# Kernel tuning notes

Hardware: AMD Instinct MI355X
Metric: run time of the kernel (lower is better)

## Reference

```python
import jax, jax.numpy as jnp
import numpy as np

N0, N1, N2 = 320000, 80000, 16000
E1, E2 = 800000, 160000
IN_C, HID, OUT_C = 128, 64, 48
H1, H2 = 4, 1
NEG_SLOPE = 0.2  # PyG GATv2Conv default leaky_relu slope


def _glorot(key, shape):
    fan_in = shape[0]
    return jax.random.normal(key, shape, jnp.float32) / jnp.sqrt(jnp.asarray(fan_in, jnp.float32))


def setup_inputs() -> dict:
    key = jax.random.key(0)
    ks = jax.random.split(key, 12)
    inp = {
        "x": jax.random.normal(ks[0], (N0, IN_C), jnp.float32),
        # layer 1: GATv2Conv(IN_C -> HID, heads=H1, concat=True)
        "Wl1": _glorot(ks[1], (IN_C, H1 * HID)),
        "bl1": jnp.zeros((H1 * HID,), jnp.float32),
        "Wr1": _glorot(ks[2], (IN_C, H1 * HID)),
        "br1": jnp.zeros((H1 * HID,), jnp.float32),
        "att1": jax.random.normal(ks[3], (H1, HID), jnp.float32) * 0.1,
        "bias1": jnp.zeros((H1 * HID,), jnp.float32),
        # layer 2: GATv2Conv(H1*HID -> OUT_C, heads=H2, concat=False)
        "Wl2": _glorot(ks[4], (H1 * HID, H2 * OUT_C)),
        "bl2": jnp.zeros((H2 * OUT_C,), jnp.float32),
        "Wr2": _glorot(ks[5], (H1 * HID, H2 * OUT_C)),
        "br2": jnp.zeros((H2 * OUT_C,), jnp.float32),
        "att2": jax.random.normal(ks[6], (H2, OUT_C), jnp.float32) * 0.1,
        "bias2": jnp.zeros((OUT_C,), jnp.float32),
        # sampled bipartite edge lists (edge j->i: src index into x_src, dst into x_dst)
        "src1": jax.random.randint(ks[7], (E1,), 0, N0, jnp.int32),
        "dst1": jax.random.randint(ks[8], (E1,), 0, N1, jnp.int32),
        "src2": jax.random.randint(ks[9], (E2,), 0, N1, jnp.int32),
        "dst2": jax.random.randint(ks[10], (E2,), 0, N2, jnp.int32),
        "n1": N1,
        "n2": N2,
    }
    return inp


def gatv2_conv(x_src, x_dst, src, dst, Wl, bl, Wr, br, att, bias, n_dst, concat):
    H, C = att.shape
    xl = (x_src @ Wl + bl).reshape(-1, H, C)   # [N_src, H, C] (source transform)
    xr = (x_dst @ Wr + br).reshape(-1, H, C)   # [N_dst, H, C] (target transform)
    e = xl[src] + xr[dst]                      # [E, H, C]
    e = jnp.where(e > 0, e, NEG_SLOPE * e)     # leaky_relu (GATv2: nonlinearity before att)
    alpha = jnp.einsum('ehc,hc->eh', e, att)   # [E, H] attention logits
    # softmax over edges sharing the same target node
    amax = jax.ops.segment_max(alpha, dst, num_segments=n_dst)
    ex = jnp.exp(alpha - amax[dst])
    denom = jax.ops.segment_sum(ex, dst, num_segments=n_dst)
    w = ex / (denom[dst] + 1e-16)              # [E, H]
    out = jax.ops.segment_sum(xl[src] * w[:, :, None], dst, num_segments=n_dst)  # [N_dst, H, C]
    out = out.reshape(n_dst, H * C) if concat else out.mean(axis=1)
    return out + bias


def reference(x, Wl1, bl1, Wr1, br1, att1, bias1, Wl2, bl2, Wr2, br2, att2, bias2,
              src1, dst1, src2, dst2, n1, n2):
    h = gatv2_conv(x, x[:n1], src1, dst1, Wl1, bl1, Wr1, br1, att1, bias1, n1, True)
    h = jax.nn.relu(h)
    # dropout is identity in eval mode
    h = gatv2_conv(h, h[:n2], src2, dst2, Wl2, bl2, Wr2, br2, att2, bias2, n2, False)
    return jax.nn.log_softmax(h, axis=-1)
```

## Files before the change

### kernel.cpp

```cpp
#include <hip/hip_runtime.h>
#include <hip/hip_bf16.h>

#define N0_  320000
#define N1_  80000
#define N2_  16000
#define INC_ 128
#define HID_ 64
#define H1_  4
#define C1_  256
#define OUT_ 48
#define OUTP_ 64
#define NEG_ 0.2f

typedef __attribute__((ext_vector_type(8))) short bfrag8;
typedef __attribute__((ext_vector_type(4))) float ffrag4;

__device__ __forceinline__ float bf2f(unsigned short u){
  unsigned int v = ((unsigned int)u) << 16;
  return __uint_as_float(v);
}
__device__ __forceinline__ unsigned short f2bf(float f){
  unsigned int u = __float_as_uint(f);
  u += 0x7FFFu + ((u >> 16) & 1u);
  return (unsigned short)(u >> 16);
}
__device__ __forceinline__ void unpack2(unsigned int u, float& lo, float& hi){
  lo = __uint_as_float(u << 16);
  hi = __uint_as_float(u & 0xffff0000u);
}

__global__ void transpose_all(const float* __restrict__ Wl1, const float* __restrict__ Wr1,
                              const float* __restrict__ Wl2, const float* __restrict__ Wr2,
                              unsigned short* __restrict__ Wt1l, unsigned short* __restrict__ Wt1r,
                              unsigned short* __restrict__ Wt2l, unsigned short* __restrict__ Wt2r){
  int idx = blockIdx.x*256 + threadIdx.x;
  if (idx < 32768){ int n = idx >> 7, k = idx & 127; Wt1l[idx] = f2bf(Wl1[k*C1_ + n]); }
  else if (idx < 65536){ int j = idx - 32768; int n = j >> 7, k = j & 127; Wt1r[j] = f2bf(Wr1[k*C1_ + n]); }
  else if (idx < 77824){ int j = idx - 65536; int n = j >> 8, k = j & 255; Wt2l[j] = f2bf(Wl2[k*OUT_ + n]); }
  else if (idx < 90112){ int j = idx - 77824; int n = j >> 8, k = j & 255; Wt2r[j] = f2bf(Wr2[k*OUT_ + n]); }
}

__global__ __launch_bounds__(256, 2) void gemm1_v4(
    const float* __restrict__ X,
    const unsigned short* __restrict__ Wtl, const unsigned short* __restrict__ Wtr,
    const float* __restrict__ bl, const float* __restrict__ br,
    unsigned short* __restrict__ outl, unsigned short* __restrict__ outr,
    int nblk_l, int tiles)
{
  __shared__ unsigned short As[64*136];
  __shared__ unsigned short Csh[32*264];
  const int t = threadIdx.x;
  const int lane = t & 63, wave = t >> 6;
  const bool isR = (int)blockIdx.x >= nblk_l;
  const int blk = isR ? (int)blockIdx.x - nblk_l : (int)blockIdx.x;
  const unsigned short* Wt = isR ? Wtr : Wtl;
  const float* bias = isR ? br : bl;
  unsigned short* out = isR ? outr : outl;
  const int l15 = lane & 15, q = lane >> 4;
  const int wcol = wave << 6;
  const int r8 = t >> 5;
  const int c32 = t & 31;

  int row0 = (blk * tiles) << 6;
  float4 pf[8];
  #pragma unroll
  for (int i = 0; i < 8; ++i)
    pf[i] = *(const float4*)(X + ((size_t)(row0 + (i<<3) + r8) << 7) + (c32<<2));

  bfrag8 bfr[4][4];
  #pragma unroll
  for (int nt = 0; nt < 4; ++nt)
    #pragma unroll
    for (int ks = 0; ks < 4; ++ks)
      bfr[nt][ks] = *(const bfrag8*)(Wt + (size_t)(wcol + (nt<<4) + l15)*128 + (ks<<5) + (q<<3));
  float bb[4];
  #pragma unroll
  for (int nt = 0; nt < 4; ++nt) bb[nt] = bias[wcol + (nt<<4) + l15];

  #pragma unroll
  for (int i = 0; i < 8; ++i){
    ushort4 s; s.x=f2bf(pf[i].x); s.y=f2bf(pf[i].y); s.z=f2bf(pf[i].z); s.w=f2bf(pf[i].w);
    *(ushort4*)(&As[((i<<3) + r8)*136 + (c32<<2)]) = s;
  }
  __syncthreads();

  for (int tile = 0; tile < tiles; ++tile){
    row0 = (blk * tiles + tile) << 6;
    const bool havenext = (tile + 1 < tiles);
    if (havenext){
      int rown = row0 + 64;
      #pragma unroll
      for (int i = 0; i < 8; ++i)
        pf[i] = *(const float4*)(X + ((size_t)(rown + (i<<3) + r8) << 7) + (c32<<2));
    }

    ffrag4 z = {0.f,0.f,0.f,0.f};
    ffrag4 acc[4][4];
    #pragma unroll
    for (int mt = 0; mt < 4; ++mt)
      #pragma unroll
      for (int nt = 0; nt < 4; ++nt) acc[mt][nt] = z;

    #pragma unroll
    for (int mt = 0; mt < 4; ++mt)
      #pragma unroll
      for (int ks = 0; ks < 4; ++ks){
        bfrag8 af = *(const bfrag8*)(&As[((mt<<4) + l15)*136 + (ks<<5) + (q<<3)]);
        #pragma unroll
        for (int nt = 0; nt < 4; ++nt)
          acc[mt][nt] = __builtin_amdgcn_mfma_f32_16x16x32_bf16(af, bfr[nt][ks], acc[mt][nt], 0, 0, 0);
      }

    __syncthreads();
    if (havenext){
      #pragma unroll
      for (int i = 0; i < 8; ++i){
        ushort4 s; s.x=f2bf(pf[i].x); s.y=f2bf(pf[i].y); s.z=f2bf(pf[i].z); s.w=f2bf(pf[i].w);
        *(ushort4*)(&As[((i<<3) + r8)*136 + (c32<<2)]) = s;
      }
    }

    #pragma unroll
    for (int h = 0; h < 2; ++h){
      if (h) __syncthreads();
      #pragma unroll
      for (int mh = 0; mh < 2; ++mh){
        int mt = (h<<1) + mh;
        #pragma unroll
        for (int nt = 0; nt < 4; ++nt)
          #pragma unroll
          for (int rg = 0; rg < 4; ++rg)
            Csh[((mh<<4) + (q<<2) + rg)*264 + wcol + (nt<<4) + l15] = f2bf(acc[mt][nt][rg] + bb[nt]);
      }
      __syncthreads();
      #pragma unroll
      for (int i = 0; i < 4; ++i){
        int idx = (i<<8) + t;
        int r = idx >> 5, c = (idx & 31) << 3;
        *(bfrag8*)(out + ((size_t)(row0 + (h<<5) + r) << 8) + c) = *(const bfrag8*)(&Csh[r*264 + c]);
      }
    }
    __syncthreads();
  }
}

__global__ __launch_bounds__(256) void gemm2_v2(
    const unsigned short* __restrict__ Hin,
    const unsigned short* __restrict__ Wtl, const unsigned short* __restrict__ Wtr,
    const float* __restrict__ bl, const float* __restrict__ br,
    float* __restrict__ outl, float* __restrict__ outr, int nblk_l)
{
  const int t = threadIdx.x;
  const int lane = t & 63, wave = t >> 6;
  const bool isR = (int)blockIdx.x >= nblk_l;
  const int row0 = (isR ? (int)blockIdx.x - nblk_l : (int)blockIdx.x) << 6;
  const unsigned short* Wt = isR ? Wtr : Wtl;
  const float* bias = isR ? br : bl;
  float* out = isR ? outr : outl;
  const int l15 = lane & 15, q = lane >> 4;

  if (wave < 3){
    bfrag8 bfr[8];
    #pragma unroll
    for (int ks = 0; ks < 8; ++ks)
      bfr[ks] = *(const bfrag8*)(Wt + (size_t)((wave<<4) + l15)*256 + (ks<<5) + (q<<3));
    ffrag4 z = {0.f,0.f,0.f,0.f};
    ffrag4 acc[4] = {z, z, z, z};
    #pragma unroll
    for (int ks = 0; ks < 8; ++ks){
      #pragma unroll
      for (int mt = 0; mt < 4; ++mt){
        bfrag8 af = *(const bfrag8*)(Hin + ((size_t)(row0 + (mt<<4) + l15) << 8) + (ks<<5) + (q<<3));
        acc[mt] = __builtin_amdgcn_mfma_f32_16x16x32_bf16(af, bfr[ks], acc[mt], 0, 0, 0);
      }
    }
    int col = (wave<<4) + l15;
    float bbv = bias[col];
    #pragma unroll
    for (int mt = 0; mt < 4; ++mt)
      #pragma unroll
      for (int rg = 0; rg < 4; ++rg){
        int row = row0 + (mt<<4) + (q<<2) + rg;
        out[(size_t)row*OUTP_ + col] = acc[mt][rg] + bbv;
      }
  } else {
    #pragma unroll
    for (int i = 0; i < 16; ++i){
      int row = row0 + (i<<2) + q;
      out[(size_t)row*OUTP_ + 48 + l15] = 0.f;
    }
  }
}

__global__ void hist_both(const int* __restrict__ dst1, const int* __restrict__ dst2,
                          int* __restrict__ cnt1, int* __restrict__ cnt2, int E1, int E2){
  int i = blockIdx.x*256 + threadIdx.x;
  if (i < E1) atomicAdd(&cnt1[dst1[i]], 1);
  else if (i < E1 + E2) atomicAdd(&cnt2[dst2[i - E1]], 1);
}

__global__ __launch_bounds__(256) void scan_local_both(
    const int* __restrict__ in1, const int* __restrict__ in2,
    int* __restrict__ ex1, int* __restrict__ ex2,
    int* __restrict__ part1, int* __restrict__ part2, int n1, int n2, int nb1){
  __shared__ int s[256];
  const int* in; int* excl; int* partials; int n; int b;
  if ((int)blockIdx.x < nb1){ in = in1; excl = ex1; partials = part1; n = n1; b = blockIdx.x; }
  else { in = in2; excl = ex2; partials = part2; n = n2; b = blockIdx.x - nb1; }
  int t = threadIdx.x, i = b*256 + t;
  int v = (i < n) ? in[i] : 0;
  s[t] = v; __syncthreads();
  #pragma unroll
  for (int off = 1; off < 256; off <<= 1){
    int u = (t >= off) ? s[t-off] : 0;
    __syncthreads();
    s[t] += u; __syncthreads();
  }
  if (i < n) excl[i] = s[t] - v;
  if (t == 255) partials[b] = s[255];
}

__global__ __launch_bounds__(512) void scan_partials_both(
    int* __restrict__ part1, int* __restrict__ part2, int nb1, int nb2){
  __shared__ int s[512];
  int* partials = blockIdx.x ? part2 : part1;
  int nb = blockIdx.x ? nb2 : nb1;
  int t = threadIdx.x;
  int v = (t < nb) ? partials[t] : 0;
  s[t] = v; __syncthreads();
  #pragma unroll
  for (int off = 1; off < 512; off <<= 1){
    int u = (t >= off) ? s[t-off] : 0;
    __syncthreads();
    s[t] += u; __syncthreads();
  }
  if (t < nb) partials[t] = s[t] - v;
}

__global__ void scan_finalize_both(
    int* __restrict__ ex1, int* __restrict__ ex2,
    const int* __restrict__ part1, const int* __restrict__ part2,
    int* __restrict__ cur1, int* __restrict__ cur2, int n1, int n2, int nb1){
  int* excl; const int* partials; int* cursor; int n; int b;
  if ((int)blockIdx.x < nb1){ excl = ex1; partials = part1; cursor = cur1; n = n1; b = blockIdx.x; }
  else { excl = ex2; partials = part2; cursor = cur2; n = n2; b = blockIdx.x - nb1; }
  int i = b*256 + threadIdx.x;
  if (i >= n) return;
  int o = excl[i] + partials[b];
  excl[i] = o; cursor[i] = o;
}

__global__ void scatter_both(const int* __restrict__ src1, const int* __restrict__ dst1,
                             const int* __restrict__ src2, const int* __restrict__ dst2,
                             int* __restrict__ cur1, int* __restrict__ cur2,
                             int* __restrict__ perm1, int* __restrict__ perm2, int E1, int E2){
  int i = blockIdx.x*256 + threadIdx.x;
  if (i < E1){
    int pos = atomicAdd(&cur1[dst1[i]], 1);
    perm1[pos] = src1[i];
  } else if (i < E1 + E2){
    int j = i - E1;
    int pos = atomicAdd(&cur2[dst2[j]], 1);
    perm2[pos] = src2[j];
  }
}

__global__ __launch_bounds__(256) void gat_aggregate1(
    const unsigned short* __restrict__ xl, const unsigned short* __restrict__ xr,
    const int* __restrict__ offsets, const int* __restrict__ counts,
    const int* __restrict__ perm, const float* __restrict__ att,
    const float* __restrict__ bias, unsigned short* __restrict__ hout, int n)
{
  int node = (blockIdx.x << 2) + (threadIdx.x >> 6);
  if (node >= n) return;
  const int lane = threadIdx.x & 63;
  const int slot = lane >> 5;
  const int sub  = lane & 31;
  const int elem = sub << 3;
  const unsigned int ebyte = (unsigned)elem << 1;
  const char* xlb = (const char*)xl;

  const int st = offsets[node], cnt = counts[node];
  uint4 ru = *(const uint4*)(xr + ((size_t)node << 8) + elem);
  float r[8];
  unpack2(ru.x, r[0], r[1]); unpack2(ru.y, r[2], r[3]);
  unpack2(ru.z, r[4], r[5]); unpack2(ru.w, r[6], r[7]);
  float4 al = *(const float4*)(att + elem);
  float4 ah = *(const float4*)(att + elem + 4);
  float a[8] = {al.x, al.y, al.z, al.w, ah.x, ah.y, ah.z, ah.w};

  float acc[8] = {0,0,0,0,0,0,0,0};
  float den = 0.f;

  for (int jb = 0; jb < cnt; jb += 64){
    int m = cnt - jb; if (m > 64) m = 64;
    int pv = (lane < m) ? perm[st + jb + lane] : 0;
    int s_cur = __shfl(pv, slot);
    uint4 xc = *(const uint4*)(xlb + (((unsigned)s_cur << 9) + ebyte));
    for (int j = 0; j < m; j += 2){
      int s_next = __shfl(pv, (j + 2 + slot) & 63);
      uint4 xn = *(const uint4*)(xlb + (((unsigned)s_next << 9) + ebyte));
      float x[8];
      unpack2(xc.x, x[0], x[1]); unpack2(xc.y, x[2], x[3]);
      unpack2(xc.z, x[4], x[5]); unpack2(xc.w, x[6], x[7]);
      float p = 0.f;
      #pragma unroll
      for (int i = 0; i < 8; ++i){
        float v = x[i] + r[i];
        float e = fmaf(NEG_, fminf(v, 0.f), fmaxf(v, 0.f));
        p = fmaf(e, a[i], p);
      }
      p += __shfl_xor(p, 1);
      p += __shfl_xor(p, 2);
      p += __shfl_xor(p, 4);
      float ex = __expf(p);
      ex = (j + slot < m) ? ex : 0.f;
      den += ex;
      #pragma unroll
      for (int i = 0; i < 8; ++i) acc[i] = fmaf(ex, x[i], acc[i]);
      xc = xn;
    }
  }
  den += __shfl_xor(den, 32);
  #pragma unroll
  for (int i = 0; i < 8; ++i) acc[i] += __shfl_xor(acc[i], 32);

  if (slot == 0){
    float w = 1.f / (den + 1e-16f);
    float4 bl = *(const float4*)(bias + elem);
    float4 bh = *(const float4*)(bias + elem + 4);
    float b[8] = {bl.x, bl.y, bl.z, bl.w, bh.x, bh.y, bh.z, bh.w};
    unsigned int o[4];
    #pragma unroll
    for (int i = 0; i < 4; ++i){
      unsigned short lo = f2bf(fmaxf(fmaf(acc[2*i],   w, b[2*i]),   0.f));
      unsigned short hi = f2bf(fmaxf(fmaf(acc[2*i+1], w, b[2*i+1]), 0.f));
      o[i] = (unsigned)lo | ((unsigned)hi << 16);
    }
    *(uint4*)(hout + ((size_t)node << 8) + elem) = make_uint4(o[0], o[1], o[2], o[3]);
  }
}

__global__ __launch_bounds__(256) void gat_aggregate2(
    const float* __restrict__ xl, const float* __restrict__ xr,
    const int* __restrict__ offsets, const int* __restrict__ counts,
    const int* __restrict__ perm, const float* __restrict__ att,
    const float* __restrict__ bias, float* __restrict__ out, int n)
{
  int node = (blockIdx.x << 2) + (threadIdx.x >> 6);
  if (node >= n) return;
  const int lane = threadIdx.x & 63;
  const int slot = lane >> 4;
  const int sub  = lane & 15;
  const bool realc = sub < 12;

  const int st = offsets[node], cnt = counts[node];
  float4 r = *(const float4*)(xr + (size_t)node*OUTP_ + (sub<<2));
  float4 a = realc ? *(const float4*)(att + (sub<<2)) : make_float4(0,0,0,0);
  float4 acc = make_float4(0,0,0,0);
  float den = 0.f;

  for (int jb = 0; jb < cnt; jb += 64){
    int m = cnt - jb; if (m > 64) m = 64;
    int pv = (lane < m) ? perm[st + jb + lane] : 0;
    int s_cur = __shfl(pv, slot);
    float4 xc = *(const float4*)(xl + (size_t)((unsigned)s_cur*OUTP_ + (sub<<2)));
    for (int j = 0; j < m; j += 4){
      int s_next = __shfl(pv, (j + 4 + slot) & 63);
      float4 xn = *(const float4*)(xl + (size_t)((unsigned)s_next*OUTP_ + (sub<<2)));
      float v0 = xc.x + r.x, v1 = xc.y + r.y, v2 = xc.z + r.z, v3 = xc.w + r.w;
      float p;
      p = fmaf(a.x, fmaf(NEG_, fminf(v0,0.f), fmaxf(v0,0.f)), 0.f);
      p = fmaf(a.y, fmaf(NEG_, fminf(v1,0.f), fmaxf(v1,0.f)), p);
      p = fmaf(a.z, fmaf(NEG_, fminf(v2,0.f), fmaxf(v2,0.f)), p);
      p = fmaf(a.w, fmaf(NEG_, fminf(v3,0.f), fmaxf(v3,0.f)), p);
      p += __shfl_xor(p, 1);
      p += __shfl_xor(p, 2);
      p += __shfl_xor(p, 4);
      p += __shfl_xor(p, 8);
      float ex = __expf(p);
      ex = (j + slot < m) ? ex : 0.f;
      den += ex;
      acc.x = fmaf(ex, xc.x, acc.x); acc.y = fmaf(ex, xc.y, acc.y);
      acc.z = fmaf(ex, xc.z, acc.z); acc.w = fmaf(ex, xc.w, acc.w);
      xc = xn;
    }
  }
  den += __shfl_xor(den, 16); den += __shfl_xor(den, 32);
  acc.x += __shfl_xor(acc.x, 16); acc.x += __shfl_xor(acc.x, 32);
  acc.y += __shfl_xor(acc.y, 16); acc.y += __shfl_xor(acc.y, 32);
  acc.z += __shfl_xor(acc.z, 16); acc.z += __shfl_xor(acc.z, 32);
  acc.w += __shfl_xor(acc.w, 16); acc.w += __shfl_xor(acc.w, 32);

  float w = 1.f / (den + 1e-16f);
  float4 b = realc ? *(const float4*)(bias + (sub<<2)) : make_float4(0,0,0,0);
  float v0 = fmaf(acc.x, w, b.x), v1 = fmaf(acc.y, w, b.y);
  float v2 = fmaf(acc.z, w, b.z), v3 = fmaf(acc.w, w, b.w);

  float mx = realc ? fmaxf(fmaxf(v0, v1), fmaxf(v2, v3)) : -3.0e38f;
  mx = fmaxf(mx, __shfl_xor(mx, 1)); mx = fmaxf(mx, __shfl_xor(mx, 2));
  mx = fmaxf(mx, __shfl_xor(mx, 4)); mx = fmaxf(mx, __shfl_xor(mx, 8));
  float es = realc ? (__expf(v0-mx) + __expf(v1-mx) + __expf(v2-mx) + __expf(v3-mx)) : 0.f;
  es += __shfl_xor(es, 1); es += __shfl_xor(es, 2);
  es += __shfl_xor(es, 4); es += __shfl_xor(es, 8);
  float ls = __logf(es);
  if (slot == 0 && realc){
    float4 o = make_float4(v0-mx-ls, v1-mx-ls, v2-mx-ls, v3-mx-ls);
    *(float4*)(out + (size_t)node*OUT_ + (sub<<2)) = o;
  }
}

extern "C" void kernel_launch(void* const* d_in, const int* in_sizes, int n_in,
                              void* d_out, int out_size, void* d_ws, size_t ws_size,
                              hipStream_t stream)
{
  const float* x    = (const float*)d_in[0];
  const float* Wl1  = (const float*)d_in[1];
  const float* bl1  = (const float*)d_in[2];
  const float* Wr1  = (const float*)d_in[3];
  const float* br1  = (const float*)d_in[4];
  const float* att1 = (const float*)d_in[5];
  const float* bias1= (const float*)d_in[6];
  const float* Wl2  = (const float*)d_in[7];
  const float* bl2  = (const float*)d_in[8];
  const float* Wr2  = (const float*)d_in[9];
  const float* br2  = (const float*)d_in[10];
  const float* att2 = (const float*)d_in[11];
  const float* bias2= (const float*)d_in[12];
  const int* src1 = (const int*)d_in[13];
  const int* dst1 = (const int*)d_in[14];
  const int* src2 = (const int*)d_in[15];
  const int* dst2 = (const int*)d_in[16];
  const int E1 = in_sizes[13];
  const int E2 = in_sizes[15];
  (void)n_in; (void)out_size; (void)ws_size;

  char* ws = (char*)d_ws;
  unsigned short* xl1  = (unsigned short*)(ws + 0LL);
  unsigned short* xr1  = (unsigned short*)(ws + 163840000LL);
  unsigned short* hbuf = (unsigned short*)(ws + 204800000LL);
  float* xl2p   = (float*)(ws + 245760000LL);
  float* xr2p   = (float*)(ws + 266240000LL);
  int*   perm1  = (int*)  (ws + 270336000LL);
  int*   perm2  = (int*)  (ws + 273536000LL);
  int*   cnt1   = (int*)  (ws + 274176000LL);
  int*   cnt2   = (int*)  (ws + 274496000LL);
  int*   off1   = (int*)  (ws + 274560000LL);
  int*   cur1   = (int*)  (ws + 274880000LL);
  int*   off2   = (int*)  (ws + 275200000LL);
  int*   cur2   = (int*)  (ws + 275264000LL);
  int*   part1  = (int*)  (ws + 275328000LL);
  int*   part2  = (int*)  (ws + 275330048LL);
  unsigned short* Wt1l = (unsigned short*)(ws + 275332096LL);
  unsigned short* Wt1r = (unsigned short*)(ws + 275397632LL);
  unsigned short* Wt2l = (unsigned short*)(ws + 275463168LL);
  unsigned short* Wt2r = (unsigned short*)(ws + 275487744LL);

  hipMemsetAsync(ws + 274176000LL, 0, 384000LL, stream);

  const int nb1 = (N1_ + 255) / 256;
  const int nb2 = (N2_ + 255) / 256;

  transpose_all<<<352, 256, 0, stream>>>(Wl1, Wr1, Wl2, Wr2, Wt1l, Wt1r, Wt2l, Wt2r);

  hist_both         <<<(E1+E2+255)/256, 256, 0, stream>>>(dst1, dst2, cnt1, cnt2, E1, E2);
  scan_local_both   <<<nb1+nb2, 256, 0, stream>>>(cnt1, cnt2, off1, off2, part1, part2, N1_, N2_, nb1);
  scan_partials_both<<<2, 512, 0, stream>>>(part1, part2, nb1, nb2);
  scan_finalize_both<<<nb1+nb2, 256, 0, stream>>>(off1, off2, part1, part2, cur1, cur2, N1_, N2_, nb1);
  scatter_both      <<<(E1+E2+255)/256, 256, 0, stream>>>(src1, dst1, src2, dst2,
                                                          cur1, cur2, perm1, perm2, E1, E2);

  gemm1_v4<<<1250, 256, 0, stream>>>(x, Wt1l, Wt1r, bl1, br1, xl1, xr1, 1000, 5);

  gat_aggregate1<<<(N1_+3)/4, 256, 0, stream>>>(xl1, xr1, off1, cnt1, perm1,
                                                att1, bias1, hbuf, N1_);

  gemm2_v2<<<N1_/64 + N2_/64, 256, 0, stream>>>(hbuf, Wt2l, Wt2r, bl2, br2, xl2p, xr2p, N1_/64);

  gat_aggregate2<<<(N2_+3)/4, 256, 0, stream>>>(xl2p, xr2p, off2, cnt2, perm2,
                                                att2, bias2, (float*)d_out, N2_);
}
```

Measured before the change: 553.5 us.

## Shrink gemm1 tile, store MFMA results directly, stage gemm2 A in LDS

gemm1 now works on 32-row tiles with twice as many blocks. The MFMA operands are swapped so each lane holds four consecutive output columns and can write bf16 results straight to global memory, which removes the shared-memory C staging and its extra barriers. gemm2 now stages the 64x256 input tile in LDS once, and each wave computes 16 rows across all 48 output columns with float4 stores, instead of three waves re-reading the input from global while one wave only writes zero padding. The cost is smaller per-block reuse in gemm1 and narrower 8-byte global stores.

```diff
diff --git a/kernel.cpp b/kernel.cpp
--- a/kernel.cpp
+++ b/kernel.cpp
@@ -40,15 +40,14 @@
   else if (idx < 90112){ int j = idx - 77824; int n = j >> 8, k = j & 255; Wt2r[j] = f2bf(Wr2[k*OUT_ + n]); }
 }
 
-__global__ __launch_bounds__(256, 2) void gemm1_v4(
+__global__ __launch_bounds__(256) void gemm1_v5(
     const float* __restrict__ X,
     const unsigned short* __restrict__ Wtl, const unsigned short* __restrict__ Wtr,
     const float* __restrict__ bl, const float* __restrict__ br,
     unsigned short* __restrict__ outl, unsigned short* __restrict__ outr,
     int nblk_l, int tiles)
 {
-  __shared__ unsigned short As[64*136];
-  __shared__ unsigned short Csh[32*264];
+  __shared__ unsigned short As[32*136];
   const int t = threadIdx.x;
   const int lane = t & 63, wave = t >> 6;
   const bool isR = (int)blockIdx.x >= nblk_l;
@@ -58,14 +57,6 @@
   unsigned short* out = isR ? outr : outl;
   const int l15 = lane & 15, q = lane >> 4;
   const int wcol = wave << 6;
-  const int r8 = t >> 5;
-  const int c32 = t & 31;
-
-  int row0 = (blk * tiles) << 6;
-  float4 pf[8];
-  #pragma unroll
-  for (int i = 0; i < 8; ++i)
-    pf[i] = *(const float4*)(X + ((size_t)(row0 + (i<<3) + r8) << 7) + (c32<<2));
 
   bfrag8 bfr[4][4];
   #pragma unroll
@@ -73,83 +64,89 @@
     #pragma unroll
     for (int ks = 0; ks < 4; ++ks)
       bfr[nt][ks] = *(const bfrag8*)(Wt + (size_t)(wcol + (nt<<4) + l15)*128 + (ks<<5) + (q<<3));
-  float bb[4];
-  #pragma unroll
-  for (int nt = 0; nt < 4; ++nt) bb[nt] = bias[wcol + (nt<<4) + l15];
-
-  #pragma unroll
-  for (int i = 0; i < 8; ++i){
+  float4 bb[4];
+  #pragma unroll
+  for (int nt = 0; nt < 4; ++nt)
+    bb[nt] = *(const float4*)(bias + wcol + (nt<<4) + (q<<2));
+
+  int row0 = (blk * tiles) << 5;
+  float4 pf[4];
+  #pragma unroll
+  for (int i = 0; i < 4; ++i){
+    int idx = (i<<8) + t;
+    pf[i] = *(const float4*)(X + ((size_t)(row0 + (idx>>5)) << 7) + ((idx&31)<<2));
+  }
+  #pragma unroll
+  for (int i = 0; i < 4; ++i){
+    int idx = (i<<8) + t;
     ushort4 s; s.x=f2bf(pf[i].x); s.y=f2bf(pf[i].y); s.z=f2bf(pf[i].z); s.w=f2bf(pf[i].w);
-    *(ushort4*)(&As[((i<<3) + r8)*136 + (c32<<2)]) = s;
+    *(ushort4*)(&As[(idx>>5)*136 + ((idx&31)<<2)]) = s;
   }
   __syncthreads();
 
   for (int tile = 0; tile < tiles; ++tile){
-    row0 = (blk * tiles + tile) << 6;
+    row0 = (blk * tiles + tile) << 5;
     const bool havenext = (tile + 1 < tiles);
     if (havenext){
-      int rown = row0 + 64;
-      #pragma unroll
-      for (int i = 0; i < 8; ++i)
-        pf[i] = *(const float4*)(X + ((size_t)(rown + (i<<3) + r8) << 7) + (c32<<2));
+      int rown = row0 + 32;
+      #pragma unroll
+      for (int i = 0; i < 4; ++i){
+        int idx = (i<<8) + t;
+        pf[i] = *(const float4*)(X + ((size_t)(rown + (idx>>5)) << 7) + ((idx&31)<<2));
+      }
     }
 
     ffrag4 z = {0.f,0.f,0.f,0.f};
-    ffrag4 acc[4][4];
-    #pragma unroll
-    for (int mt = 0; mt < 4; ++mt)
+    ffrag4 acc[2][4];
+    #pragma unroll
+    for (int mt = 0; mt < 2; ++mt)
       #pragma unroll
       for (int nt = 0; nt < 4; ++nt) acc[mt][nt] = z;
 
     #pragma unroll
-    for (int mt = 0; mt < 4; ++mt)
+    for (int mt = 0; mt < 2; ++mt)
       #pragma unroll
       for (int ks = 0; ks < 4; ++ks){
         bfrag8 af = *(const bfrag8*)(&As[((mt<<4) + l15)*136 + (ks<<5) + (q<<3)]);
         #pragma unroll
         for (int nt = 0; nt < 4; ++nt)
-          acc[mt][nt] = __builtin_amdgcn_mfma_f32_16x16x32_bf16(af, bfr[nt][ks], acc[mt][nt], 0, 0, 0);
+          acc[mt][nt] = __builtin_amdgcn_mfma_f32_16x16x32_bf16(bfr[nt][ks], af, acc[mt][nt], 0, 0, 0);
       }
+
+    #pragma unroll
+    for (int mt = 0; mt < 2; ++mt){
+      int row = row0 + (mt<<4) + l15;
+      #pragma unroll
+      for (int nt = 0; nt < 4; ++nt){
+        ushort4 s;
+        s.x = f2bf(acc[mt][nt][0] + bb[nt].x);
+        s.y = f2bf(acc[mt][nt][1] + bb[nt].y);
+        s.z = f2bf(acc[mt][nt][2] + bb[nt].z);
+        s.w = f2bf(acc[mt][nt][3] + bb[nt].w);
+        *(ushort4*)(out + ((size_t)row << 8) + wcol + (nt<<4) + (q<<2)) = s;
+      }
+    }
 
     __syncthreads();
     if (havenext){
       #pragma unroll
-      for (int i = 0; i < 8; ++i){
+      for (int i = 0; i < 4; ++i){
+        int idx = (i<<8) + t;
         ushort4 s; s.x=f2bf(pf[i].x); s.y=f2bf(pf[i].y); s.z=f2bf(pf[i].z); s.w=f2bf(pf[i].w);
-        *(ushort4*)(&As[((i<<3) + r8)*136 + (c32<<2)]) = s;
-      }
-    }
-
-    #pragma unroll
-    for (int h = 0; h < 2; ++h){
-      if (h) __syncthreads();
-      #pragma unroll
-      for (int mh = 0; mh < 2; ++mh){
-        int mt = (h<<1) + mh;
-        #pragma unroll
-        for (int nt = 0; nt < 4; ++nt)
-          #pragma unroll
-          for (int rg = 0; rg < 4; ++rg)
-            Csh[((mh<<4) + (q<<2) + rg)*264 + wcol + (nt<<4) + l15] = f2bf(acc[mt][nt][rg] + bb[nt]);
+        *(ushort4*)(&As[(idx>>5)*136 + ((idx&31)<<2)]) = s;
       }
       __syncthreads();
-      #pragma unroll
-      for (int i = 0; i < 4; ++i){
-        int idx = (i<<8) + t;
-        int r = idx >> 5, c = (idx & 31) << 3;
-        *(bfrag8*)(out + ((size_t)(row0 + (h<<5) + r) << 8) + c) = *(const bfrag8*)(&Csh[r*264 + c]);
-      }
-    }
-    __syncthreads();
-  }
-}
-
-__global__ __launch_bounds__(256) void gemm2_v2(
+    }
+  }
+}
+
+__global__ __launch_bounds__(256) void gemm2_v3(
     const unsigned short* __restrict__ Hin,
     const unsigned short* __restrict__ Wtl, const unsigned short* __restrict__ Wtr,
     const float* __restrict__ bl, const float* __restrict__ br,
     float* __restrict__ outl, float* __restrict__ outr, int nblk_l)
 {
+  __shared__ unsigned short As2[64*264];
   const int t = threadIdx.x;
   const int lane = t & 63, wave = t >> 6;
   const bool isR = (int)blockIdx.x >= nblk_l;
@@ -159,37 +156,36 @@
   float* out = isR ? outr : outl;
   const int l15 = lane & 15, q = lane >> 4;
 
-  if (wave < 3){
-    bfrag8 bfr[8];
-    #pragma unroll
-    for (int ks = 0; ks < 8; ++ks)
-      bfr[ks] = *(const bfrag8*)(Wt + (size_t)((wave<<4) + l15)*256 + (ks<<5) + (q<<3));
-    ffrag4 z = {0.f,0.f,0.f,0.f};
-    ffrag4 acc[4] = {z, z, z, z};
-    #pragma unroll
-    for (int ks = 0; ks < 8; ++ks){
-      #pragma unroll
-      for (int mt = 0; mt < 4; ++mt){
-        bfrag8 af = *(const bfrag8*)(Hin + ((size_t)(row0 + (mt<<4) + l15) << 8) + (ks<<5) + (q<<3));
-        acc[mt] = __builtin_amdgcn_mfma_f32_16x16x32_bf16(af, bfr[ks], acc[mt], 0, 0, 0);
-      }
-    }
-    int col = (wave<<4) + l15;
-    float bbv = bias[col];
-    #pragma unroll
-    for (int mt = 0; mt < 4; ++mt)
-      #pragma unroll
-      for (int rg = 0; rg < 4; ++rg){
-        int row = row0 + (mt<<4) + (q<<2) + rg;
-        out[(size_t)row*OUTP_ + col] = acc[mt][rg] + bbv;
-      }
-  } else {
-    #pragma unroll
-    for (int i = 0; i < 16; ++i){
-      int row = row0 + (i<<2) + q;
-      out[(size_t)row*OUTP_ + 48 + l15] = 0.f;
-    }
-  }
+  #pragma unroll
+  for (int i = 0; i < 8; ++i){
+    int idx = (i<<8) + t;
+    int r = idx >> 5, c = (idx & 31) << 3;
+    *(bfrag8*)(&As2[r*264 + c]) = *(const bfrag8*)(Hin + ((size_t)(row0 + r) << 8) + c);
+  }
+  __syncthreads();
+
+  ffrag4 z = {0.f,0.f,0.f,0.f};
+  ffrag4 acc[3] = {z, z, z};
+  #pragma unroll
+  for (int ks = 0; ks < 8; ++ks){
+    bfrag8 af = *(const bfrag8*)(&As2[((wave<<4) + l15)*264 + (ks<<5) + (q<<3)]);
+    #pragma unroll
+    for (int nt = 0; nt < 3; ++nt){
+      bfrag8 bf = *(const bfrag8*)(Wt + (size_t)((nt<<4) + l15)*256 + (ks<<5) + (q<<3));
+      acc[nt] = __builtin_amdgcn_mfma_f32_16x16x32_bf16(bf, af, acc[nt], 0, 0, 0);
+    }
+  }
+
+  int row = row0 + (wave<<4) + l15;
+  #pragma unroll
+  for (int nt = 0; nt < 3; ++nt){
+    float4 b4 = *(const float4*)(bias + (nt<<4) + (q<<2));
+    float4 o;
+    o.x = acc[nt][0] + b4.x; o.y = acc[nt][1] + b4.y;
+    o.z = acc[nt][2] + b4.z; o.w = acc[nt][3] + b4.w;
+    *(float4*)(out + (size_t)row*OUTP_ + (nt<<4) + (q<<2)) = o;
+  }
+  *(float4*)(out + (size_t)row*OUTP_ + 48 + (q<<2)) = make_float4(0.f,0.f,0.f,0.f);
 }
 
 __global__ void hist_both(const int* __restrict__ dst1, const int* __restrict__ dst2,
@@ -470,12 +466,12 @@
   scatter_both      <<<(E1+E2+255)/256, 256, 0, stream>>>(src1, dst1, src2, dst2,
                                                           cur1, cur2, perm1, perm2, E1, E2);
 
-  gemm1_v4<<<1250, 256, 0, stream>>>(x, Wt1l, Wt1r, bl1, br1, xl1, xr1, 1000, 5);
+  gemm1_v5<<<2500, 256, 0, stream>>>(x, Wt1l, Wt1r, bl1, br1, xl1, xr1, 2000, 5);
 
   gat_aggregate1<<<(N1_+3)/4, 256, 0, stream>>>(xl1, xr1, off1, cnt1, perm1,
                                                 att1, bias1, hbuf, N1_);
 
-  gemm2_v2<<<N1_/64 + N2_/64, 256, 0, stream>>>(hbuf, Wt2l, Wt2r, bl2, br2, xl2p, xr2p, N1_/64);
+  gemm2_v3<<<N1_/64 + N2_/64, 256, 0, stream>>>(hbuf, Wt2l, Wt2r, bl2, br2, xl2p, xr2p, N1_/64);
 
   gat_aggregate2<<<(N2_+3)/4, 256, 0, stream>>>(xl2p, xr2p, off2, cnt2, perm2,
                                                 att2, bias2, (float*)d_out, N2_);
```

Result: no change. 555.6 us (+0.4%).
